# Kernel tuning notes

Hardware: AMD Instinct MI355X
Metric: run time of the kernel (lower is better)

Reference implementation:

```python
import jax, jax.numpy as jnp
import numpy as np

B, F, K, DEPTH = 512, 64, 64, 3  # feas == k == 64, deepDepth == 3


def setup_inputs() -> dict:
    key = jax.random.key(0)
    ks = jax.random.split(key, 16)
    x = jax.random.normal(ks[0], (B, F), dtype=jnp.float32)
    # wide: Linear(feas, 1)
    Ww = jax.random.normal(ks[1], (1, F), dtype=jnp.float32) * 0.1
    bw = jnp.zeros((1,), dtype=jnp.float32)
    # cross: Parameter(torch.rand(feas, k))
    cross = jax.random.uniform(ks[2], (F, K), dtype=jnp.float32)
    # attention: Linear(k, k) -> ReLU -> Linear(k, 1, bias=False)
    W1 = jax.random.normal(ks[3], (K, K), dtype=jnp.float32) / np.sqrt(K)
    b1 = jnp.zeros((K,), dtype=jnp.float32)
    w2 = jax.random.normal(ks[4], (K,), dtype=jnp.float32) / np.sqrt(K)
    # deep{i}: Linear(k//i, k//(i+1)) + ReLU, i = 1..DEPTH  -> 64->32->21->16
    dims = [K // i for i in range(1, DEPTH + 2)]  # [64, 32, 21, 16]
    Wd1 = jax.random.normal(ks[5], (dims[1], dims[0]), dtype=jnp.float32) / np.sqrt(dims[0])
    bd1 = jnp.zeros((dims[1],), dtype=jnp.float32)
    Wd2 = jax.random.normal(ks[6], (dims[2], dims[1]), dtype=jnp.float32) / np.sqrt(dims[1])
    bd2 = jnp.zeros((dims[2],), dtype=jnp.float32)
    Wd3 = jax.random.normal(ks[7], (dims[3], dims[2]), dtype=jnp.float32) / np.sqrt(dims[2])
    bd3 = jnp.zeros((dims[3],), dtype=jnp.float32)
    # out: Linear(feas // (deepDepth+1), 1) == Linear(16, 1)
    Wo = jax.random.normal(ks[8], (1, F // (DEPTH + 1)), dtype=jnp.float32) * 0.1
    bo = jnp.zeros((1,), dtype=jnp.float32)
    return {"x": x, "Ww": Ww, "bw": bw, "cross": cross, "W1": W1, "b1": b1,
            "w2": w2, "Wd1": Wd1, "bd1": bd1, "Wd2": Wd2, "bd2": bd2,
            "Wd3": Wd3, "bd3": bd3, "Wo": Wo, "bo": bo}


def reference(x, Ww, bw, cross, W1, b1, w2, Wd1, bd1, Wd2, bd2, Wd3, bd3, Wo, bo):
    linear = x @ Ww.T + bw  # [B, 1]

    # Pairwise FM interactions v[b,i,j,:] = x_i * x_j * (cross_i ∘ cross_j)
    xx = x[:, :, None] * x[:, None, :]                    # [B, F, F]
    cp = cross[:, None, :] * cross[None, :, :]            # [F, F, K]
    v = xx[..., None] * cp[None]                          # [B, F, F, K]

    # attention MLP score per pair
    h = jax.nn.relu(jnp.einsum('bijk,lk->bijl', v, W1) + b1)
    s = jnp.einsum('bijl,l->bij', h, w2)                  # [B, F, F]

    # loop semantics: upper triangle (j >= i), pair kept iff x_i != 0 and x_j != 0
    valid = jnp.triu(jnp.ones((F, F), dtype=bool))[None] \
        & (x[:, :, None] != 0) & (x[:, None, :] != 0)     # [B, F, F]
    neg = jnp.finfo(s.dtype).min
    logits = jnp.where(valid, s, neg)

    # softmax over [0 (seed zeros(1) entry), valid pair scores...];
    # the seed zeros(k) value-vector contributes nothing to the weighted sum.
    m = jnp.maximum(jnp.max(logits, axis=(1, 2)), 0.0)    # [B]
    e = jnp.where(valid, jnp.exp(logits - m[:, None, None]), 0.0)
    denom = jnp.exp(-m) + jnp.sum(e, axis=(1, 2))         # +exp(-m) is the 0-logit term
    tmp = jnp.einsum('bij,bijk->bk', e, v) / denom[:, None]  # [B, K]

    tmp = jax.nn.relu(tmp @ Wd1.T + bd1)
    tmp = jax.nn.relu(tmp @ Wd2.T + bd2)
    tmp = jax.nn.relu(tmp @ Wd3.T + bd3)
    deep_out = tmp @ Wo.T + bo                            # [B, 1]
    return jax.nn.sigmoid(linear + deep_out)
```

## Files before the change

### kernel.cpp

```cpp
#include <hip/hip_runtime.h>
#include <math.h>


#define BB 512
#define FF 64
#define STR 68
#define NPAIRS 2080
#define THREADS 512
#define NIT2 65
#define NEG_BIG -3.402823466e38f

typedef _Float16 half8 __attribute__((ext_vector_type(8)));
typedef _Float16 half4 __attribute__((ext_vector_type(4)));
typedef float f32x4 __attribute__((ext_vector_type(4)));

__device__ __forceinline__ half8 ld8(const _Float16* p) {
    half8 v;
    *(half4*)&v       = *(const half4*)p;
    *((half4*)&v + 1) = *(const half4*)(p + 4);
    return v;
}

__global__ __launch_bounds__(THREADS, 4) void afm_r5_kernel(
    const float* __restrict__ x,
    const float* __restrict__ Ww,
    const float* __restrict__ bw,
    const float* __restrict__ cross,
    const float* __restrict__ W1,
    const float* __restrict__ b1,
    const float* __restrict__ w2,
    const float* __restrict__ Wd1,
    const float* __restrict__ bd1,
    const float* __restrict__ Wd2,
    const float* __restrict__ bd2,
    const float* __restrict__ Wd3,
    const float* __restrict__ bd3,
    const float* __restrict__ Wo,
    const float* __restrict__ bo,
    float* __restrict__ out)
{
    __shared__ __align__(16) _Float16 ah_s [FF * STR];
    __shared__ __align__(16) _Float16 aht_s[FF * STR];
    __shared__ __align__(16) _Float16 M_s  [FF * STR];
    __shared__ float s_s[NPAIRS];
    __shared__ unsigned short lut_s[NPAIRS];
    __shared__ float x_sh[FF];
    __shared__ float part_s[4][FF];
    __shared__ float mlp_s[FF];
    __shared__ float red_s[16];

    const int tid  = threadIdx.x;
    const int lane = tid & 63;
    const int wave = tid >> 6;
    const int b    = blockIdx.x;
    const int m    = lane & 15;
    const int q    = lane >> 4;

    if (tid < FF) x_sh[tid] = x[b * FF + tid];
    __syncthreads();

    for (int idx = tid; idx < FF * FF; idx += THREADS) {
        const int i = idx >> 6, k = idx & 63;
        const _Float16 v = (_Float16)(x_sh[i] * cross[idx]);
        ah_s[i * STR + k]  = v;
        aht_s[k * STR + i] = v;
    }
    for (int idx = tid; idx < (FF * STR) / 2; idx += THREADS)
        ((int*)M_s)[idx] = 0;
    if (tid < FF) {
        const int i = tid;
        const int basei = i * FF - (i * (i - 1)) / 2;
        const bool xi = (x_sh[i] != 0.f);
        for (int j = i; j < FF; ++j) {
            const int valid = (xi && (x_sh[j] != 0.f)) ? 0x8000 : 0;
            lut_s[basei + (j - i)] = (unsigned short)((i << 8) | j | valid);
        }
    }

    half8 afr[4][2];
    #pragma unroll
    for (int mt = 0; mt < 4; ++mt)
        #pragma unroll
        for (int kt = 0; kt < 2; ++kt) {
            const float* wr = W1 + (mt * 16 + m) * FF + kt * 32 + q * 8;
            half8 h;
            #pragma unroll
            for (int jj = 0; jj < 8; ++jj) h[jj] = (_Float16)wr[jj];
            afr[mt][kt] = h;
        }
    float b1r[16], w2r[16];
    #pragma unroll
    for (int mt = 0; mt < 4; ++mt)
        #pragma unroll
        for (int r = 0; r < 4; ++r) {
            b1r[mt * 4 + r] = b1[mt * 16 + q * 4 + r];
            w2r[mt * 4 + r] = w2[mt * 16 + q * 4 + r];
        }
    __syncthreads();

    for (int it = wave; it < NIT2; it += 8) {
        const int p0 = it * 32;
        const int ijA = lut_s[p0 + m];
        const int ijB = lut_s[p0 + 16 + m];
        const int iA = (ijA >> 8) & 63, jA = ijA & 63;
        const int iB = (ijB >> 8) & 63, jB = ijB & 63;
        const half8 bA0 = ld8(&ah_s[iA * STR + q * 8])      * ld8(&ah_s[jA * STR + q * 8]);
        const half8 bA1 = ld8(&ah_s[iA * STR + 32 + q * 8]) * ld8(&ah_s[jA * STR + 32 + q * 8]);
        const half8 bB0 = ld8(&ah_s[iB * STR + q * 8])      * ld8(&ah_s[jB * STR + q * 8]);
        const half8 bB1 = ld8(&ah_s[iB * STR + 32 + q * 8]) * ld8(&ah_s[jB * STR + 32 + q * 8]);
        float spA = 0.f, spB = 0.f;
        #pragma unroll
        for (int mt = 0; mt < 4; ++mt) {
            f32x4 aA, aB;
            #pragma unroll
            for (int r = 0; r < 4; ++r) { aA[r] = b1r[mt * 4 + r]; aB[r] = b1r[mt * 4 + r]; }
            aA = __builtin_amdgcn_mfma_f32_16x16x32_f16(afr[mt][0], bA0, aA, 0, 0, 0);
            aB = __builtin_amdgcn_mfma_f32_16x16x32_f16(afr[mt][0], bB0, aB, 0, 0, 0);
            aA = __builtin_amdgcn_mfma_f32_16x16x32_f16(afr[mt][1], bA1, aA, 0, 0, 0);
            aB = __builtin_amdgcn_mfma_f32_16x16x32_f16(afr[mt][1], bB1, aB, 0, 0, 0);
            #pragma unroll
            for (int r = 0; r < 4; ++r) {
                spA = fmaf(w2r[mt * 4 + r], fmaxf(aA[r], 0.f), spA);
                spB = fmaf(w2r[mt * 4 + r], fmaxf(aB[r], 0.f), spB);
            }
        }
        spA += __shfl_xor(spA, 16, 64);
        spA += __shfl_xor(spA, 32, 64);
        spB += __shfl_xor(spB, 16, 64);
        spB += __shfl_xor(spB, 32, 64);
        if (lane < 16) {
            s_s[p0 + lane]      = (ijA & 0x8000) ? spA : NEG_BIG;
            s_s[p0 + 16 + lane] = (ijB & 0x8000) ? spB : NEG_BIG;
        }
    }
    __syncthreads();

    float mx = 0.0f;
    for (int p = tid; p < NPAIRS; p += THREADS) mx = fmaxf(mx, s_s[p]);
    #pragma unroll
    for (int off = 32; off > 0; off >>= 1)
        mx = fmaxf(mx, __shfl_xor(mx, off, 64));
    if (lane == 0) red_s[wave] = mx;
    __syncthreads();
    float mval = red_s[0];
    #pragma unroll
    for (int w = 1; w < 8; ++w) mval = fmaxf(mval, red_s[w]);

    float sum = 0.f;
    for (int p = tid; p < NPAIRS; p += THREADS) {
        const int ij = lut_s[p];
        const float e = __expf(s_s[p] - mval);
        sum += e;
        M_s[((ij >> 8) & 63) * STR + (ij & 63)] = (_Float16)e;
    }
    #pragma unroll
    for (int off = 32; off > 0; off >>= 1)
        sum += __shfl_xor(sum, off, 64);
    if (lane == 0) red_s[8 + wave] = sum;
    __syncthreads();
    float denom = __expf(-mval);
    #pragma unroll
    for (int w = 0; w < 8; ++w) denom += red_s[8 + w];

    {
        const int t0 = wave * 2;
        #pragma unroll
        for (int t = t0; t < t0 + 2; ++t) {
            const int i0 = (t >> 2) * 16, k0 = (t & 3) * 16;
            const half8 a0  = ld8(&M_s[(i0 + m) * STR + q * 8]);
            const half8 a1  = ld8(&M_s[(i0 + m) * STR + 32 + q * 8]);
            const half8 bb0 = ld8(&aht_s[(k0 + m) * STR + q * 8]);
            const half8 bb1 = ld8(&aht_s[(k0 + m) * STR + 32 + q * 8]);
            f32x4 g = {0.f, 0.f, 0.f, 0.f};
            g = __builtin_amdgcn_mfma_f32_16x16x32_f16(a0, bb0, g, 0, 0, 0);
            g = __builtin_amdgcn_mfma_f32_16x16x32_f16(a1, bb1, g, 0, 0, 0);
            const half4 ap = *(const half4*)&aht_s[(k0 + m) * STR + i0 + q * 4];
            float s4 = (float)ap[0] * g[0] + (float)ap[1] * g[1]
                     + (float)ap[2] * g[2] + (float)ap[3] * g[3];
            s4 += __shfl_xor(s4, 16, 64);
            s4 += __shfl_xor(s4, 32, 64);
            if (lane < 16) part_s[i0 >> 4][k0 + lane] = s4;
        }
    }
    __syncthreads();
    if (tid < FF)
        mlp_s[tid] = (part_s[0][tid] + part_s[1][tid] +
                      part_s[2][tid] + part_s[3][tid]) / denom;
    __syncthreads();

    float hv = 0.f;
    if (tid < 32) {
        float a1v = bd1[tid];
        for (int k = 0; k < 64; ++k) a1v = fmaf(Wd1[tid * 64 + k], mlp_s[k], a1v);
        hv = fmaxf(a1v, 0.f);
    }
    __syncthreads();
    if (tid < 32) mlp_s[tid] = hv;
    __syncthreads();
    if (tid < 21) {
        float a2 = bd2[tid];
        for (int k = 0; k < 32; ++k) a2 = fmaf(Wd2[tid * 32 + k], mlp_s[k], a2);
        hv = fmaxf(a2, 0.f);
    }
    __syncthreads();
    if (tid < 21) mlp_s[tid] = hv;
    __syncthreads();
    if (tid < 16) {
        float a3 = bd3[tid];
        for (int k = 0; k < 21; ++k) a3 = fmaf(Wd3[tid * 21 + k], mlp_s[k], a3);
        hv = fmaxf(a3, 0.f);
    }
    __syncthreads();
    if (tid < 16) mlp_s[tid] = hv;
    __syncthreads();

    if (tid == 0) {
        float deep = bo[0];
        for (int k = 0; k < 16; ++k) deep = fmaf(Wo[k], mlp_s[k], deep);
        float lin = bw[0];
        for (int k = 0; k < 64; ++k) lin = fmaf(Ww[k], x_sh[k], lin);
        const float z = lin + deep;
        out[b] = 1.f / (1.f + __expf(-z));
    }
}

extern "C" void kernel_launch(void* const* d_in, const int* in_sizes, int n_in,
                              void* d_out, int out_size, void* d_ws, size_t ws_size,
                              hipStream_t stream) {
    const float* xp    = (const float*)d_in[0];
    const float* Ww    = (const float*)d_in[1];
    const float* bw    = (const float*)d_in[2];
    const float* cross = (const float*)d_in[3];
    const float* W1    = (const float*)d_in[4];
    const float* b1    = (const float*)d_in[5];
    const float* w2    = (const float*)d_in[6];
    const float* Wd1   = (const float*)d_in[7];
    const float* bd1   = (const float*)d_in[8];
    const float* Wd2   = (const float*)d_in[9];
    const float* bd2   = (const float*)d_in[10];
    const float* Wd3   = (const float*)d_in[11];
    const float* bd3   = (const float*)d_in[12];
    const float* Wo    = (const float*)d_in[13];
    const float* bo    = (const float*)d_in[14];
    float* outp = (float*)d_out;

    afm_r5_kernel<<<BB, THREADS, 0, stream>>>(xp, Ww, bw, cross, W1, b1, w2,
                                              Wd1, bd1, Wd2, bd2, Wd3, bd3,
                                              Wo, bo, outp);
}
```

Measured before the change: 103.3 us.

## Replace pair LUT with row-based tiling in attention score loop

Removes the shared-memory pair lookup table and its serial construction, and instead assigns each wave fixed rows i, tiling j in groups of 16 with the row-i operand loaded once per row. The pair index and the validity mask are computed arithmetically. The aim is to drop the LUT build and indirect loads, at the cost of some padded MFMA work on partial tiles and a softmax loop that now skips half its indices.

```diff
diff --git a/kernel.cpp b/kernel.cpp
--- a/kernel.cpp
+++ b/kernel.cpp
@@ -7,7 +7,6 @@
 #define STR 68
 #define NPAIRS 2080
 #define THREADS 512
-#define NIT2 65
 #define NEG_BIG -3.402823466e38f
 
 typedef _Float16 half8 __attribute__((ext_vector_type(8)));
@@ -21,7 +20,7 @@
     return v;
 }
 
-__global__ __launch_bounds__(THREADS, 4) void afm_r5_kernel(
+__global__ __launch_bounds__(THREADS, 4) void afm_r6_kernel(
     const float* __restrict__ x,
     const float* __restrict__ Ww,
     const float* __restrict__ bw,
@@ -43,7 +42,6 @@
     __shared__ __align__(16) _Float16 aht_s[FF * STR];
     __shared__ __align__(16) _Float16 M_s  [FF * STR];
     __shared__ float s_s[NPAIRS];
-    __shared__ unsigned short lut_s[NPAIRS];
     __shared__ float x_sh[FF];
     __shared__ float part_s[4][FF];
     __shared__ float mlp_s[FF];
@@ -67,15 +65,6 @@
     }
     for (int idx = tid; idx < (FF * STR) / 2; idx += THREADS)
         ((int*)M_s)[idx] = 0;
-    if (tid < FF) {
-        const int i = tid;
-        const int basei = i * FF - (i * (i - 1)) / 2;
-        const bool xi = (x_sh[i] != 0.f);
-        for (int j = i; j < FF; ++j) {
-            const int valid = (xi && (x_sh[j] != 0.f)) ? 0x8000 : 0;
-            lut_s[basei + (j - i)] = (unsigned short)((i << 8) | j | valid);
-        }
-    }
 
     half8 afr[4][2];
     #pragma unroll
@@ -98,39 +87,38 @@
         }
     __syncthreads();
 
-    for (int it = wave; it < NIT2; it += 8) {
-        const int p0 = it * 32;
-        const int ijA = lut_s[p0 + m];
-        const int ijB = lut_s[p0 + 16 + m];
-        const int iA = (ijA >> 8) & 63, jA = ijA & 63;
-        const int iB = (ijB >> 8) & 63, jB = ijB & 63;
-        const half8 bA0 = ld8(&ah_s[iA * STR + q * 8])      * ld8(&ah_s[jA * STR + q * 8]);
-        const half8 bA1 = ld8(&ah_s[iA * STR + 32 + q * 8]) * ld8(&ah_s[jA * STR + 32 + q * 8]);
-        const half8 bB0 = ld8(&ah_s[iB * STR + q * 8])      * ld8(&ah_s[jB * STR + q * 8]);
-        const half8 bB1 = ld8(&ah_s[iB * STR + 32 + q * 8]) * ld8(&ah_s[jB * STR + 32 + q * 8]);
-        float spA = 0.f, spB = 0.f;
-        #pragma unroll
-        for (int mt = 0; mt < 4; ++mt) {
-            f32x4 aA, aB;
+    #pragma unroll
+    for (int g = 0; g < 8; ++g) {
+        const int i = wave + 8 * g;
+        const int nt = 4 - (g >> 1);
+        const int basei = i * FF - (i * (i - 1)) / 2;
+        const float xi = x_sh[i];
+        const half8 ai0 = ld8(&ah_s[i * STR + q * 8]);
+        const half8 ai1 = ld8(&ah_s[i * STR + 32 + q * 8]);
+        #pragma unroll
+        for (int t = 0; t < nt; ++t) {
+            const int j0 = i + 16 * t;
+            const int jc = min(j0 + m, 63);
+            const half8 bf0 = ai0 * ld8(&ah_s[jc * STR + q * 8]);
+            const half8 bf1 = ai1 * ld8(&ah_s[jc * STR + 32 + q * 8]);
+            const float xjv = x_sh[jc];
+            float sp = 0.f;
             #pragma unroll
-            for (int r = 0; r < 4; ++r) { aA[r] = b1r[mt * 4 + r]; aB[r] = b1r[mt * 4 + r]; }
-            aA = __builtin_amdgcn_mfma_f32_16x16x32_f16(afr[mt][0], bA0, aA, 0, 0, 0);
-            aB = __builtin_amdgcn_mfma_f32_16x16x32_f16(afr[mt][0], bB0, aB, 0, 0, 0);
-            aA = __builtin_amdgcn_mfma_f32_16x16x32_f16(afr[mt][1], bA1, aA, 0, 0, 0);
-            aB = __builtin_amdgcn_mfma_f32_16x16x32_f16(afr[mt][1], bB1, aB, 0, 0, 0);
-            #pragma unroll
-            for (int r = 0; r < 4; ++r) {
-                spA = fmaf(w2r[mt * 4 + r], fmaxf(aA[r], 0.f), spA);
-                spB = fmaf(w2r[mt * 4 + r], fmaxf(aB[r], 0.f), spB);
+            for (int mt = 0; mt < 4; ++mt) {
+                f32x4 acc;
+                #pragma unroll
+                for (int r = 0; r < 4; ++r) acc[r] = b1r[mt * 4 + r];
+                acc = __builtin_amdgcn_mfma_f32_16x16x32_f16(afr[mt][0], bf0, acc, 0, 0, 0);
+                acc = __builtin_amdgcn_mfma_f32_16x16x32_f16(afr[mt][1], bf1, acc, 0, 0, 0);
+                #pragma unroll
+                for (int r = 0; r < 4; ++r)
+                    sp = fmaf(w2r[mt * 4 + r], fmaxf(acc[r], 0.f), sp);
             }
-        }
-        spA += __shfl_xor(spA, 16, 64);
-        spA += __shfl_xor(spA, 32, 64);
-        spB += __shfl_xor(spB, 16, 64);
-        spB += __shfl_xor(spB, 32, 64);
-        if (lane < 16) {
-            s_s[p0 + lane]      = (ijA & 0x8000) ? spA : NEG_BIG;
-            s_s[p0 + 16 + lane] = (ijB & 0x8000) ? spB : NEG_BIG;
+            sp += __shfl_xor(sp, 16, 64);
+            sp += __shfl_xor(sp, 32, 64);
+            const bool valid = (xi != 0.f) && (xjv != 0.f);
+            if (lane < 16 && (j0 + lane) < FF)
+                s_s[basei + 16 * t + lane] = valid ? sp : NEG_BIG;
         }
     }
     __syncthreads();
@@ -147,11 +135,14 @@
     for (int w = 1; w < 8; ++w) mval = fmaxf(mval, red_s[w]);
 
     float sum = 0.f;
-    for (int p = tid; p < NPAIRS; p += THREADS) {
-        const int ij = lut_s[p];
-        const float e = __expf(s_s[p] - mval);
-        sum += e;
-        M_s[((ij >> 8) & 63) * STR + (ij & 63)] = (_Float16)e;
+    for (int idx = tid; idx < FF * FF; idx += THREADS) {
+        const int i = idx >> 6, j = idx & 63;
+        if (j >= i) {
+            const int p = i * FF - (i * (i - 1)) / 2 + (j - i);
+            const float e = __expf(s_s[p] - mval);
+            sum += e;
+            M_s[i * STR + j] = (_Float16)e;
+        }
     }
     #pragma unroll
     for (int off = 32; off > 0; off >>= 1)
@@ -171,12 +162,12 @@
             const half8 a1  = ld8(&M_s[(i0 + m) * STR + 32 + q * 8]);
             const half8 bb0 = ld8(&aht_s[(k0 + m) * STR + q * 8]);
             const half8 bb1 = ld8(&aht_s[(k0 + m) * STR + 32 + q * 8]);
-            f32x4 g = {0.f, 0.f, 0.f, 0.f};
-            g = __builtin_amdgcn_mfma_f32_16x16x32_f16(a0, bb0, g, 0, 0, 0);
-            g = __builtin_amdgcn_mfma_f32_16x16x32_f16(a1, bb1, g, 0, 0, 0);
+            f32x4 gacc = {0.f, 0.f, 0.f, 0.f};
+            gacc = __builtin_amdgcn_mfma_f32_16x16x32_f16(a0, bb0, gacc, 0, 0, 0);
+            gacc = __builtin_amdgcn_mfma_f32_16x16x32_f16(a1, bb1, gacc, 0, 0, 0);
             const half4 ap = *(const half4*)&aht_s[(k0 + m) * STR + i0 + q * 4];
-            float s4 = (float)ap[0] * g[0] + (float)ap[1] * g[1]
-                     + (float)ap[2] * g[2] + (float)ap[3] * g[3];
+            float s4 = (float)ap[0] * gacc[0] + (float)ap[1] * gacc[1]
+                     + (float)ap[2] * gacc[2] + (float)ap[3] * gacc[3];
             s4 += __shfl_xor(s4, 16, 64);
             s4 += __shfl_xor(s4, 32, 64);
             if (lane < 16) part_s[i0 >> 4][k0 + lane] = s4;
@@ -244,7 +235,7 @@
     const float* bo    = (const float*)d_in[14];
     float* outp = (float*)d_out;
 
-    afm_r5_kernel<<<BB, THREADS, 0, stream>>>(xp, Ww, bw, cross, W1, b1, w2,
+    afm_r6_kernel<<<BB, THREADS, 0, stream>>>(xp, Ww, bw, cross, W1, b1, w2,
                                               Wd1, bd1, Wd2, bd2, Wd3, bd3,
                                               Wo, bo, outp);
 }
```

Measured after the change: 104.6 us. About the same (+1.3%).
